# Optimization experiments

Measured on AMD Instinct MI355X. Metric: run time of the kernel, lower is better.

Reference implementation:

```python
import jax, jax.numpy as jnp
import numpy as np

B, CIN, COUT, H, W, K = 4, 3, 16, 256, 256, 5
PAD = K // 2  # replicate padding keeps spatial size


def _dilation_sum(x, w):
    """Learnable dilation, channel_merge_mode='sum'.
    x: (B,Cin,H,W), w: (Cout,Cin,K,K).
    out[b,o,i,j] = sum_c max_{di,dj} ( x_pad[b,c,i+di,j+dj] + w[o,c,di,dj] )
    """
    xp = jnp.pad(x, ((0, 0), (0, 0), (PAD, PAD), (PAD, PAD)), mode='edge')
    acc = jnp.full((x.shape[0], w.shape[0], x.shape[1], H, W), -jnp.inf, dtype=x.dtype)
    for di in range(K):  # fixed small kernel loop (unrolled), not a data-dim loop
        for dj in range(K):
            win = xp[:, :, di:di + H, dj:dj + W]                     # (B,Cin,H,W)
            cand = win[:, None] + w[None, :, :, di, dj][:, :, :, None, None]  # (B,Cout,Cin,H,W)
            acc = jnp.maximum(acc, cand)
    return acc.sum(axis=2)  # merge over input channels -> (B,Cout,H,W)


def _erosion_identity(y, w):
    """Learnable erosion, channel_merge_mode='identity' (each channel independent).
    y: (B,Cout,H,W), w: (Cout,K,K).
    out[b,o,i,j] = min_{di,dj} ( y_pad[b,o,i+di,j+dj] - w[o,di,dj] )
    """
    yp = jnp.pad(y, ((0, 0), (0, 0), (PAD, PAD), (PAD, PAD)), mode='edge')
    acc = jnp.full(y.shape, jnp.inf, dtype=y.dtype)
    for di in range(K):
        for dj in range(K):
            acc = jnp.minimum(acc, yp[:, :, di:di + H, dj:dj + W] - w[None, :, di, dj, None, None])
    return acc


def setup_inputs() -> dict:
    key = jax.random.key(0)
    k1, k2, k3 = jax.random.split(key, 3)
    x = jax.random.normal(k1, (B, CIN, H, W), dtype=jnp.float32)
    w_d = jax.random.normal(k2, (COUT, CIN, K, K), dtype=jnp.float32) * 0.05
    w_e = jax.random.normal(k3, (COUT, K, K), dtype=jnp.float32) * 0.05
    return {"x": x, "w_d": w_d, "w_e": w_e}


def reference(x, w_d, w_e):
    # Closing = dilation (max-plus, sum merge) followed by erosion (min-plus, identity merge)
    dilated = _dilation_sum(x, w_d)
    return _erosion_identity(dilated, w_e)
```

## Files before the change

kernel.cpp:

```cpp
#include <hip/hip_runtime.h>


namespace {
constexpr int Hh = 256, Ww = 256;
constexpr int CI = 3, CO = 16;
constexpr int TILE = 32;
constexpr int DT = 36;
constexpr int XT = 40;
}

__global__ __launch_bounds__(256, 4)
void closing_fused(const float* __restrict__ x, const float* __restrict__ wd,
                   const float* __restrict__ we, float* __restrict__ out) {
    __shared__ __align__(16) float sx[CI * XT * XT];
    __shared__ __align__(16) float sdil[DT * DT];

    const int tid = threadIdx.x;
    const int bx = blockIdx.x, by = blockIdx.y, z = blockIdx.z;
    const int o = z & 15;
    const int i0 = by * TILE, j0 = bx * TILE;

    const float* xb  = x + (size_t)(z >> 4) * (CI * Hh * Ww);
    const float* wdo = wd + o * (CI * 25);
    const float* weo = we + o * 25;

    for (int idx = tid; idx < CI * XT * XT; idx += 256) {
        const int c   = idx / (XT * XT);
        const int rem = idx - c * (XT * XT);
        const int r   = rem / XT;
        const int col = rem - r * XT;
        int gi = i0 - 4 + r;   gi = min(max(gi, 0), Hh - 1);
        int gj = j0 - 4 + col; gj = min(max(gj, 0), Ww - 1);
        sx[idx] = xb[c * (Hh * Ww) + gi * Ww + gj];
    }
    __syncthreads();

    for (int task = tid; task < DT * (DT / 4); task += 256) {
        const int tr = task / 9;
        const int tj = (task - tr * 9) * 4;
        float acc0 = 0.f, acc1 = 0.f, acc2 = 0.f, acc3 = 0.f;
#pragma unroll
        for (int c = 0; c < CI; ++c) {
            float win[5][8];
#pragma unroll
            for (int dd = 0; dd < 5; ++dd) {
                const float4 a  = *(const float4*)&sx[c*(XT*XT) + (tr+dd)*XT + tj];
                const float4 bq = *(const float4*)&sx[c*(XT*XT) + (tr+dd)*XT + tj + 4];
                win[dd][0]=a.x;  win[dd][1]=a.y;  win[dd][2]=a.z;  win[dd][3]=a.w;
                win[dd][4]=bq.x; win[dd][5]=bq.y; win[dd][6]=bq.z; win[dd][7]=bq.w;
            }
            float m0 = -3.402823e38f, m1 = m0, m2 = m0, m3 = m0;
#pragma unroll
            for (int dd = 0; dd < 5; ++dd) {
#pragma unroll
                for (int d2 = 0; d2 < 5; ++d2) {
                    const float wv = wdo[c*25 + dd*5 + d2];
                    m0 = fmaxf(m0, win[dd][d2+0] + wv);
                    m1 = fmaxf(m1, win[dd][d2+1] + wv);
                    m2 = fmaxf(m2, win[dd][d2+2] + wv);
                    m3 = fmaxf(m3, win[dd][d2+3] + wv);
                }
            }
            acc0 += m0; acc1 += m1; acc2 += m2; acc3 += m3;
        }
        *(float4*)&sdil[tr * DT + tj] = make_float4(acc0, acc1, acc2, acc3);
    }
    __syncthreads();

    const int r  = tid >> 3;
    const int oj = (tid & 7) * 4;
    float win[5][8];
    const bool interior = (bx != 0) & (bx != (Ww / TILE - 1)) &
                          (by != 0) & (by != (Hh / TILE - 1));
    if (interior) {
#pragma unroll
        for (int dd = 0; dd < 5; ++dd) {
            const float4 a  = *(const float4*)&sdil[(r+dd)*DT + oj];
            const float4 bq = *(const float4*)&sdil[(r+dd)*DT + oj + 4];
            win[dd][0]=a.x;  win[dd][1]=a.y;  win[dd][2]=a.z;  win[dd][3]=a.w;
            win[dd][4]=bq.x; win[dd][5]=bq.y; win[dd][6]=bq.z; win[dd][7]=bq.w;
        }
    } else {
        int lj[8];
#pragma unroll
        for (int m = 0; m < 8; ++m) {
            int g = j0 + oj + m - 2; g = min(max(g, 0), Ww - 1);
            lj[m] = g - j0 + 2;
        }
#pragma unroll
        for (int dd = 0; dd < 5; ++dd) {
            int g = i0 + r + dd - 2; g = min(max(g, 0), Hh - 1);
            const int li = g - i0 + 2;
#pragma unroll
            for (int m = 0; m < 8; ++m) win[dd][m] = sdil[li * DT + lj[m]];
        }
    }
    float r0 = 3.402823e38f, r1 = r0, r2 = r0, r3 = r0;
#pragma unroll
    for (int dd = 0; dd < 5; ++dd) {
#pragma unroll
        for (int d2 = 0; d2 < 5; ++d2) {
            const float wv = weo[dd*5 + d2];
            r0 = fminf(r0, win[dd][d2+0] - wv);
            r1 = fminf(r1, win[dd][d2+1] - wv);
            r2 = fminf(r2, win[dd][d2+2] - wv);
            r3 = fminf(r3, win[dd][d2+3] - wv);
        }
    }
    *(float4*)&out[((size_t)z << 16) + ((i0 + r) << 8) + (j0 + oj)] =
        make_float4(r0, r1, r2, r3);
}

extern "C" void kernel_launch(void* const* d_in, const int* in_sizes, int n_in,
                              void* d_out, int out_size, void* d_ws, size_t ws_size,
                              hipStream_t stream) {
    const float* x  = (const float*)d_in[0];
    const float* wd = (const float*)d_in[1];
    const float* we = (const float*)d_in[2];
    float* out = (float*)d_out;

    dim3 grid(Ww / TILE, Hh / TILE, 4 * CO);
    closing_fused<<<grid, dim3(256), 0, stream>>>(x, wd, we, out);
}
```

Baseline: 99.49 us.

## Widen tiles to 64x32, stream input channels, and precompute replicate borders in shared memory

Tiles become 64 columns by 32 rows, which cuts halo overhead. Input channels are loaded into shared memory one at a time instead of all three at once, which lowers shared-memory use and raises the occupancy hint to 6 blocks. Each thread now produces 8 dilation outputs per row. Replicate padding for the erosion is written into the dilated tile up front, so the separate clamped-index boundary path goes away. The costs are extra syncs per channel, higher register pressure from the 8-wide accumulators, and intricate edge-fixup logic.

```diff
diff --git a/kernel.cpp b/kernel.cpp
--- a/kernel.cpp
+++ b/kernel.cpp
@@ -1,114 +1,179 @@
 #include <hip/hip_runtime.h>
+#include <float.h>
 
 
 namespace {
-constexpr int Hh = 256, Ww = 256;
-constexpr int CI = 3, CO = 16;
-constexpr int TILE = 32;
-constexpr int DT = 36;
-constexpr int XT = 40;
+constexpr int HH = 256, WW = 256;
+constexpr int CI = 3;
+constexpr int TW = 64, TH = 32;
+constexpr int DW = 68, DH = 36;
+constexpr int XW = 76, XH = 40;
 }
 
-__global__ __launch_bounds__(256, 4)
-void closing_fused(const float* __restrict__ x, const float* __restrict__ wd,
-                   const float* __restrict__ we, float* __restrict__ out) {
-    __shared__ __align__(16) float sx[CI * XT * XT];
-    __shared__ __align__(16) float sdil[DT * DT];
+__global__ __launch_bounds__(256, 6)
+void closing_v2(const float* __restrict__ x, const float* __restrict__ wd,
+                const float* __restrict__ we, float* __restrict__ out) {
+    __shared__ __align__(16) float sx[XH * XW];
+    __shared__ __align__(16) float sdil[DH * DW];
 
     const int tid = threadIdx.x;
     const int bx = blockIdx.x, by = blockIdx.y, z = blockIdx.z;
-    const int o = z & 15;
-    const int i0 = by * TILE, j0 = bx * TILE;
+    const int o = z & 15, b = z >> 4;
+    const int i0 = by * TH, j0 = bx * TW;
+    const float* xb = x + (size_t)b * (CI * HH * WW);
 
-    const float* xb  = x + (size_t)(z >> 4) * (CI * Hh * Ww);
-    const float* wdo = wd + o * (CI * 25);
-    const float* weo = we + o * 25;
+    const int r0 = tid / 9, s0 = tid - r0 * 9;
+    const int t2 = tid + 256;
+    const int r1 = t2 / 9, s1 = t2 - r1 * 9;
+    const bool has2 = (t2 < DH * 9);
 
-    for (int idx = tid; idx < CI * XT * XT; idx += 256) {
-        const int c   = idx / (XT * XT);
-        const int rem = idx - c * (XT * XT);
-        const int r   = rem / XT;
-        const int col = rem - r * XT;
-        int gi = i0 - 4 + r;   gi = min(max(gi, 0), Hh - 1);
-        int gj = j0 - 4 + col; gj = min(max(gj, 0), Ww - 1);
-        sx[idx] = xb[c * (Hh * Ww) + gi * Ww + gj];
+    float acc0[8], acc1[8];
+#pragma unroll
+    for (int j = 0; j < 8; ++j) { acc0[j] = 0.f; acc1[j] = 0.f; }
+
+    for (int c = 0; c < CI; ++c) {
+        {
+            const float* xc = xb + c * (HH * WW);
+            int rs = tid / XW, cs = tid - rs * XW;
+#pragma unroll
+            for (int k = 0; k < 12; ++k) {
+                const int idx = tid + k * 256;
+                if (idx < XH * XW) {
+                    int gi = i0 - 4 + rs; gi = min(max(gi, 0), HH - 1);
+                    int gj = j0 - 4 + cs; gj = min(max(gj, 0), WW - 1);
+                    sx[idx] = xc[(gi << 8) + gj];
+                }
+                cs += 256 - 3 * XW;
+                rs += 3;
+                if (cs >= XW) { cs -= XW; rs += 1; }
+            }
+        }
+        __syncthreads();
+
+        const float* wr = wd + (o * CI + c) * 25;
+
+        {
+            float m[8];
+#pragma unroll
+            for (int j = 0; j < 8; ++j) m[j] = -FLT_MAX;
+#pragma unroll
+            for (int dd = 0; dd < 5; ++dd) {
+                const float* p = &sx[(r0 + dd) * XW + 8 * s0];
+                const float4 a  = *(const float4*)p;
+                const float4 bq = *(const float4*)(p + 4);
+                const float4 cq = *(const float4*)(p + 8);
+                const float win[12] = {a.x,a.y,a.z,a.w, bq.x,bq.y,bq.z,bq.w,
+                                       cq.x,cq.y,cq.z,cq.w};
+                const float w0 = wr[dd*5+0], w1 = wr[dd*5+1], w2 = wr[dd*5+2],
+                            w3 = wr[dd*5+3], w4 = wr[dd*5+4];
+#pragma unroll
+                for (int j = 0; j < 8; ++j) {
+                    m[j] = fmaxf(fmaxf(m[j], win[j]   + w0), win[j+1] + w1);
+                    m[j] = fmaxf(fmaxf(m[j], win[j+2] + w2), win[j+3] + w3);
+                    m[j] = fmaxf(m[j], win[j+4] + w4);
+                }
+            }
+#pragma unroll
+            for (int j = 0; j < 8; ++j) acc0[j] += m[j];
+        }
+        if (has2) {
+            float m[8];
+#pragma unroll
+            for (int j = 0; j < 8; ++j) m[j] = -FLT_MAX;
+#pragma unroll
+            for (int dd = 0; dd < 5; ++dd) {
+                const float* p = &sx[(r1 + dd) * XW + 8 * s1];
+                const float4 a  = *(const float4*)p;
+                const float4 bq = *(const float4*)(p + 4);
+                const float4 cq = *(const float4*)(p + 8);
+                const float win[12] = {a.x,a.y,a.z,a.w, bq.x,bq.y,bq.z,bq.w,
+                                       cq.x,cq.y,cq.z,cq.w};
+                const float w0 = wr[dd*5+0], w1 = wr[dd*5+1], w2 = wr[dd*5+2],
+                            w3 = wr[dd*5+3], w4 = wr[dd*5+4];
+#pragma unroll
+                for (int j = 0; j < 8; ++j) {
+                    m[j] = fmaxf(fmaxf(m[j], win[j]   + w0), win[j+1] + w1);
+                    m[j] = fmaxf(fmaxf(m[j], win[j+2] + w2), win[j+3] + w3);
+                    m[j] = fmaxf(m[j], win[j+4] + w4);
+                }
+            }
+#pragma unroll
+            for (int j = 0; j < 8; ++j) acc1[j] += m[j];
+        }
+        if (c < CI - 1) __syncthreads();
+    }
+
+    {
+        {
+            int r = r0, s = s0;
+            if (bx == 0 && s == 0) { acc0[0] = acc0[1] = acc0[2]; }
+            if (bx == 3 && s == 8) { acc0[2] = acc0[3] = acc0[1]; }
+            const bool shadow = (by == 0 && r < 2) || (by == 7 && r > 33);
+            if (!shadow) {
+                const float4 q0 = make_float4(acc0[0], acc0[1], acc0[2], acc0[3]);
+                const float4 q1 = make_float4(acc0[4], acc0[5], acc0[6], acc0[7]);
+                float* bp = &sdil[r * DW + 8 * s];
+                *(float4*)bp = q0; if (s < 8) *(float4*)(bp + 4) = q1;
+                if (by == 0 && r == 2) {
+                    *(float4*)&sdil[0*DW + 8*s] = q0; if (s<8) *(float4*)&sdil[0*DW + 8*s + 4] = q1;
+                    *(float4*)&sdil[1*DW + 8*s] = q0; if (s<8) *(float4*)&sdil[1*DW + 8*s + 4] = q1;
+                }
+                if (by == 7 && r == 33) {
+                    *(float4*)&sdil[34*DW + 8*s] = q0; if (s<8) *(float4*)&sdil[34*DW + 8*s + 4] = q1;
+                    *(float4*)&sdil[35*DW + 8*s] = q0; if (s<8) *(float4*)&sdil[35*DW + 8*s + 4] = q1;
+                }
+            }
+        }
+        if (has2) {
+            int r = r1, s = s1;
+            if (bx == 0 && s == 0) { acc1[0] = acc1[1] = acc1[2]; }
+            if (bx == 3 && s == 8) { acc1[2] = acc1[3] = acc1[1]; }
+            const bool shadow = (by == 0 && r < 2) || (by == 7 && r > 33);
+            if (!shadow) {
+                const float4 q0 = make_float4(acc1[0], acc1[1], acc1[2], acc1[3]);
+                const float4 q1 = make_float4(acc1[4], acc1[5], acc1[6], acc1[7]);
+                float* bp = &sdil[r * DW + 8 * s];
+                *(float4*)bp = q0; if (s < 8) *(float4*)(bp + 4) = q1;
+                if (by == 0 && r == 2) {
+                    *(float4*)&sdil[0*DW + 8*s] = q0; if (s<8) *(float4*)&sdil[0*DW + 8*s + 4] = q1;
+                    *(float4*)&sdil[1*DW + 8*s] = q0; if (s<8) *(float4*)&sdil[1*DW + 8*s + 4] = q1;
+                }
+                if (by == 7 && r == 33) {
+                    *(float4*)&sdil[34*DW + 8*s] = q0; if (s<8) *(float4*)&sdil[34*DW + 8*s + 4] = q1;
+                    *(float4*)&sdil[35*DW + 8*s] = q0; if (s<8) *(float4*)&sdil[35*DW + 8*s + 4] = q1;
+                }
+            }
+        }
     }
     __syncthreads();
 
-    for (int task = tid; task < DT * (DT / 4); task += 256) {
-        const int tr = task / 9;
-        const int tj = (task - tr * 9) * 4;
-        float acc0 = 0.f, acc1 = 0.f, acc2 = 0.f, acc3 = 0.f;
+    {
+        const int er = tid >> 3, es = tid & 7;
+        const float* ew = we + o * 25;
+        float rm[8];
 #pragma unroll
-        for (int c = 0; c < CI; ++c) {
-            float win[5][8];
-#pragma unroll
-            for (int dd = 0; dd < 5; ++dd) {
-                const float4 a  = *(const float4*)&sx[c*(XT*XT) + (tr+dd)*XT + tj];
-                const float4 bq = *(const float4*)&sx[c*(XT*XT) + (tr+dd)*XT + tj + 4];
-                win[dd][0]=a.x;  win[dd][1]=a.y;  win[dd][2]=a.z;  win[dd][3]=a.w;
-                win[dd][4]=bq.x; win[dd][5]=bq.y; win[dd][6]=bq.z; win[dd][7]=bq.w;
-            }
-            float m0 = -3.402823e38f, m1 = m0, m2 = m0, m3 = m0;
-#pragma unroll
-            for (int dd = 0; dd < 5; ++dd) {
-#pragma unroll
-                for (int d2 = 0; d2 < 5; ++d2) {
-                    const float wv = wdo[c*25 + dd*5 + d2];
-                    m0 = fmaxf(m0, win[dd][d2+0] + wv);
-                    m1 = fmaxf(m1, win[dd][d2+1] + wv);
-                    m2 = fmaxf(m2, win[dd][d2+2] + wv);
-                    m3 = fmaxf(m3, win[dd][d2+3] + wv);
-                }
-            }
-            acc0 += m0; acc1 += m1; acc2 += m2; acc3 += m3;
-        }
-        *(float4*)&sdil[tr * DT + tj] = make_float4(acc0, acc1, acc2, acc3);
-    }
-    __syncthreads();
-
-    const int r  = tid >> 3;
-    const int oj = (tid & 7) * 4;
-    float win[5][8];
-    const bool interior = (bx != 0) & (bx != (Ww / TILE - 1)) &
-                          (by != 0) & (by != (Hh / TILE - 1));
-    if (interior) {
+        for (int j = 0; j < 8; ++j) rm[j] = FLT_MAX;
 #pragma unroll
         for (int dd = 0; dd < 5; ++dd) {
-            const float4 a  = *(const float4*)&sdil[(r+dd)*DT + oj];
-            const float4 bq = *(const float4*)&sdil[(r+dd)*DT + oj + 4];
-            win[dd][0]=a.x;  win[dd][1]=a.y;  win[dd][2]=a.z;  win[dd][3]=a.w;
-            win[dd][4]=bq.x; win[dd][5]=bq.y; win[dd][6]=bq.z; win[dd][7]=bq.w;
+            const float* p = &sdil[(er + dd) * DW + 8 * es];
+            const float4 a  = *(const float4*)p;
+            const float4 bq = *(const float4*)(p + 4);
+            const float4 cq = *(const float4*)(p + 8);
+            const float win[12] = {a.x,a.y,a.z,a.w, bq.x,bq.y,bq.z,bq.w,
+                                   cq.x,cq.y,cq.z,cq.w};
+            const float e0 = ew[dd*5+0], e1 = ew[dd*5+1], e2 = ew[dd*5+2],
+                        e3 = ew[dd*5+3], e4 = ew[dd*5+4];
+#pragma unroll
+            for (int j = 0; j < 8; ++j) {
+                rm[j] = fminf(fminf(rm[j], win[j]   - e0), win[j+1] - e1);
+                rm[j] = fminf(fminf(rm[j], win[j+2] - e2), win[j+3] - e3);
+                rm[j] = fminf(rm[j], win[j+4] - e4);
+            }
         }
-    } else {
-        int lj[8];
-#pragma unroll
-        for (int m = 0; m < 8; ++m) {
-            int g = j0 + oj + m - 2; g = min(max(g, 0), Ww - 1);
-            lj[m] = g - j0 + 2;
-        }
-#pragma unroll
-        for (int dd = 0; dd < 5; ++dd) {
-            int g = i0 + r + dd - 2; g = min(max(g, 0), Hh - 1);
-            const int li = g - i0 + 2;
-#pragma unroll
-            for (int m = 0; m < 8; ++m) win[dd][m] = sdil[li * DT + lj[m]];
-        }
+        float* op = &out[((size_t)z << 16) + ((size_t)(i0 + er) << 8) + j0 + 8 * es];
+        *(float4*)op       = make_float4(rm[0], rm[1], rm[2], rm[3]);
+        *(float4*)(op + 4) = make_float4(rm[4], rm[5], rm[6], rm[7]);
     }
-    float r0 = 3.402823e38f, r1 = r0, r2 = r0, r3 = r0;
-#pragma unroll
-    for (int dd = 0; dd < 5; ++dd) {
-#pragma unroll
-        for (int d2 = 0; d2 < 5; ++d2) {
-            const float wv = weo[dd*5 + d2];
-            r0 = fminf(r0, win[dd][d2+0] - wv);
-            r1 = fminf(r1, win[dd][d2+1] - wv);
-            r2 = fminf(r2, win[dd][d2+2] - wv);
-            r3 = fminf(r3, win[dd][d2+3] - wv);
-        }
-    }
-    *(float4*)&out[((size_t)z << 16) + ((i0 + r) << 8) + (j0 + oj)] =
-        make_float4(r0, r1, r2, r3);
 }
 
 extern "C" void kernel_launch(void* const* d_in, const int* in_sizes, int n_in,
@@ -119,6 +184,6 @@
     const float* we = (const float*)d_in[2];
     float* out = (float*)d_out;
 
-    dim3 grid(Ww / TILE, Hh / TILE, 4 * CO);
-    closing_fused<<<grid, dim3(256), 0, stream>>>(x, wd, we, out);
+    dim3 grid(WW / TW, HH / TH, 4 * 16);
+    closing_v2<<<grid, dim3(256), 0, stream>>>(x, wd, we, out);
 }
```

After: 170.8 us. 71.7% more time.

## Use 4x4 register tiles for dilation and fold edge replication into stores

Applied to the files above, without the earlier changes.

The dilation stage now has each of 81 threads compute a 4x4 output block, reading 8 shared-memory rows once and reusing them across four output rows instead of reloading a 5x8 window per row. The erosion's replicate-padding branch is removed by writing clamped duplicate values into the dilated tile's border cells during the dilation store. Erosion is done by 128 threads producing 8 outputs each. Shared-memory row strides are padded to 44. The cost is that only 81 and 128 of 256 threads are busy in the two compute stages, which lowers parallelism per block.

```diff
diff --git a/kernel.cpp b/kernel.cpp
--- a/kernel.cpp
+++ b/kernel.cpp
@@ -1,114 +1,125 @@
 #include <hip/hip_runtime.h>
+#include <float.h>
 
 
 namespace {
-constexpr int Hh = 256, Ww = 256;
-constexpr int CI = 3, CO = 16;
-constexpr int TILE = 32;
-constexpr int DT = 36;
-constexpr int XT = 40;
+constexpr int HH = 256, WW = 256, CI = 3;
+constexpr int TT = 32;
+constexpr int DS = 44;
+constexpr int XS = 44;
+constexpr int XR = 40;
+constexpr int XCH = XR * XS;
+}
+
+__device__ __forceinline__ float4 dapp(float4 m, float4 A, float4 B,
+                                       float w0, float w1, float w2, float w3, float w4) {
+    m.x = fmaxf(fmaxf(fmaxf(m.x, A.x + w0), fmaxf(A.y + w1, A.z + w2)), fmaxf(A.w + w3, B.x + w4));
+    m.y = fmaxf(fmaxf(fmaxf(m.y, A.y + w0), fmaxf(A.z + w1, A.w + w2)), fmaxf(B.x + w3, B.y + w4));
+    m.z = fmaxf(fmaxf(fmaxf(m.z, A.z + w0), fmaxf(A.w + w1, B.x + w2)), fmaxf(B.y + w3, B.z + w4));
+    m.w = fmaxf(fmaxf(fmaxf(m.w, A.w + w0), fmaxf(B.x + w1, B.y + w2)), fmaxf(B.z + w3, B.w + w4));
+    return m;
+}
+
+__device__ __forceinline__ void add4(float4& a, float4 m) {
+    a.x += m.x; a.y += m.y; a.z += m.z; a.w += m.w;
 }
 
 __global__ __launch_bounds__(256, 4)
-void closing_fused(const float* __restrict__ x, const float* __restrict__ wd,
-                   const float* __restrict__ we, float* __restrict__ out) {
-    __shared__ __align__(16) float sx[CI * XT * XT];
-    __shared__ __align__(16) float sdil[DT * DT];
+void closing_v3(const float* __restrict__ x, const float* __restrict__ wd,
+                const float* __restrict__ we, float* __restrict__ out) {
+    __shared__ __align__(16) float sx[CI * XCH];
+    __shared__ __align__(16) float sdil[36 * DS];
 
     const int tid = threadIdx.x;
     const int bx = blockIdx.x, by = blockIdx.y, z = blockIdx.z;
-    const int o = z & 15;
-    const int i0 = by * TILE, j0 = bx * TILE;
+    const int o = z & 15, b = z >> 4;
+    const int i0 = by * TT, j0 = bx * TT;
+    const float* xb = x + (size_t)b * (CI * HH * WW);
 
-    const float* xb  = x + (size_t)(z >> 4) * (CI * Hh * Ww);
-    const float* wdo = wd + o * (CI * 25);
-    const float* weo = we + o * 25;
-
-    for (int idx = tid; idx < CI * XT * XT; idx += 256) {
-        const int c   = idx / (XT * XT);
-        const int rem = idx - c * (XT * XT);
-        const int r   = rem / XT;
-        const int col = rem - r * XT;
-        int gi = i0 - 4 + r;   gi = min(max(gi, 0), Hh - 1);
-        int gj = j0 - 4 + col; gj = min(max(gj, 0), Ww - 1);
-        sx[idx] = xb[c * (Hh * Ww) + gi * Ww + gj];
+#pragma unroll
+    for (int k = 0; k < 19; ++k) {
+        const int idx = tid + (k << 8);
+        if (idx < CI * XR * XR) {
+            const int c   = idx / 1600;
+            const int rem = idx - c * 1600;
+            const int rr  = rem / 40;
+            const int cc  = rem - rr * 40;
+            int gi = i0 - 4 + rr; gi = min(max(gi, 0), HH - 1);
+            int gj = j0 - 4 + cc; gj = min(max(gj, 0), WW - 1);
+            sx[c * XCH + rr * XS + cc] = xb[c * (HH * WW) + (gi << 8) + gj];
+        }
     }
     __syncthreads();
 
-    for (int task = tid; task < DT * (DT / 4); task += 256) {
-        const int tr = task / 9;
-        const int tj = (task - tr * 9) * 4;
-        float acc0 = 0.f, acc1 = 0.f, acc2 = 0.f, acc3 = 0.f;
+    if (tid < 81) {
+        const int q = tid / 9, s = tid - q * 9;
+        float4 acc0 = {0,0,0,0}, acc1 = acc0, acc2 = acc0, acc3 = acc0;
 #pragma unroll
         for (int c = 0; c < CI; ++c) {
-            float win[5][8];
+            const float* wr = wd + (o * CI + c) * 25;
+            const float* base = &sx[c * XCH + (4 * q) * XS + 4 * s];
+            const float NEG = -FLT_MAX;
+            float4 m0 = {NEG,NEG,NEG,NEG}, m1 = m0, m2 = m0, m3 = m0;
 #pragma unroll
-            for (int dd = 0; dd < 5; ++dd) {
-                const float4 a  = *(const float4*)&sx[c*(XT*XT) + (tr+dd)*XT + tj];
-                const float4 bq = *(const float4*)&sx[c*(XT*XT) + (tr+dd)*XT + tj + 4];
-                win[dd][0]=a.x;  win[dd][1]=a.y;  win[dd][2]=a.z;  win[dd][3]=a.w;
-                win[dd][4]=bq.x; win[dd][5]=bq.y; win[dd][6]=bq.z; win[dd][7]=bq.w;
+            for (int dd = 0; dd < 8; ++dd) {
+                const float4 A = *(const float4*)(base + dd * XS);
+                const float4 B = *(const float4*)(base + dd * XS + 4);
+                if (dd <= 4)           m0 = dapp(m0, A, B, wr[dd*5+0], wr[dd*5+1], wr[dd*5+2], wr[dd*5+3], wr[dd*5+4]);
+                if (dd >= 1 && dd <= 5){ const int k2 = dd-1;
+                                       m1 = dapp(m1, A, B, wr[k2*5+0], wr[k2*5+1], wr[k2*5+2], wr[k2*5+3], wr[k2*5+4]); }
+                if (dd >= 2 && dd <= 6){ const int k2 = dd-2;
+                                       m2 = dapp(m2, A, B, wr[k2*5+0], wr[k2*5+1], wr[k2*5+2], wr[k2*5+3], wr[k2*5+4]); }
+                if (dd >= 3)           { const int k2 = dd-3;
+                                       m3 = dapp(m3, A, B, wr[k2*5+0], wr[k2*5+1], wr[k2*5+2], wr[k2*5+3], wr[k2*5+4]); }
             }
-            float m0 = -3.402823e38f, m1 = m0, m2 = m0, m3 = m0;
-#pragma unroll
-            for (int dd = 0; dd < 5; ++dd) {
-#pragma unroll
-                for (int d2 = 0; d2 < 5; ++d2) {
-                    const float wv = wdo[c*25 + dd*5 + d2];
-                    m0 = fmaxf(m0, win[dd][d2+0] + wv);
-                    m1 = fmaxf(m1, win[dd][d2+1] + wv);
-                    m2 = fmaxf(m2, win[dd][d2+2] + wv);
-                    m3 = fmaxf(m3, win[dd][d2+3] + wv);
-                }
-            }
-            acc0 += m0; acc1 += m1; acc2 += m2; acc3 += m3;
+            add4(acc0, m0); add4(acc1, m1); add4(acc2, m2); add4(acc3, m3);
         }
-        *(float4*)&sdil[tr * DT + tj] = make_float4(acc0, acc1, acc2, acc3);
+
+        if (bx == 0 && s == 0) {
+            acc0.x = acc0.y = acc0.z;  acc1.x = acc1.y = acc1.z;
+            acc2.x = acc2.y = acc2.z;  acc3.x = acc3.y = acc3.z;
+        }
+        if (bx == 7 && s == 8) {
+            acc0.z = acc0.w = acc0.y;  acc1.z = acc1.w = acc1.y;
+            acc2.z = acc2.w = acc2.y;  acc3.z = acc3.w = acc3.y;
+        }
+        float4 w0 = acc0, w1 = acc1, w2 = acc2, w3 = acc3;
+        if (by == 0 && q == 0) { w0 = acc2; w1 = acc2; }
+        if (by == 7 && q == 8) { w2 = acc1; w3 = acc1; }
+        float* dp = &sdil[(4 * q) * DS + 4 * s];
+        *(float4*)(dp)          = w0;
+        *(float4*)(dp + DS)     = w1;
+        *(float4*)(dp + 2 * DS) = w2;
+        *(float4*)(dp + 3 * DS) = w3;
     }
     __syncthreads();
 
-    const int r  = tid >> 3;
-    const int oj = (tid & 7) * 4;
-    float win[5][8];
-    const bool interior = (bx != 0) & (bx != (Ww / TILE - 1)) &
-                          (by != 0) & (by != (Hh / TILE - 1));
-    if (interior) {
+    if (tid < 128) {
+        const int s = tid & 3, r = tid >> 2;
+        const float* ew = we + o * 25;
+        const float* eb = &sdil[r * DS + 8 * s];
+        const float PF = FLT_MAX;
+        float4 r0 = {PF,PF,PF,PF}, r1 = r0;
 #pragma unroll
         for (int dd = 0; dd < 5; ++dd) {
-            const float4 a  = *(const float4*)&sdil[(r+dd)*DT + oj];
-            const float4 bq = *(const float4*)&sdil[(r+dd)*DT + oj + 4];
-            win[dd][0]=a.x;  win[dd][1]=a.y;  win[dd][2]=a.z;  win[dd][3]=a.w;
-            win[dd][4]=bq.x; win[dd][5]=bq.y; win[dd][6]=bq.z; win[dd][7]=bq.w;
+            const float4 A = *(const float4*)(eb + dd * DS);
+            const float4 B = *(const float4*)(eb + dd * DS + 4);
+            const float4 C = *(const float4*)(eb + dd * DS + 8);
+            const float e0 = ew[dd*5+0], e1 = ew[dd*5+1], e2 = ew[dd*5+2],
+                        e3 = ew[dd*5+3], e4 = ew[dd*5+4];
+            r0.x = fminf(fminf(fminf(r0.x, A.x - e0), fminf(A.y - e1, A.z - e2)), fminf(A.w - e3, B.x - e4));
+            r0.y = fminf(fminf(fminf(r0.y, A.y - e0), fminf(A.z - e1, A.w - e2)), fminf(B.x - e3, B.y - e4));
+            r0.z = fminf(fminf(fminf(r0.z, A.z - e0), fminf(A.w - e1, B.x - e2)), fminf(B.y - e3, B.z - e4));
+            r0.w = fminf(fminf(fminf(r0.w, A.w - e0), fminf(B.x - e1, B.y - e2)), fminf(B.z - e3, B.w - e4));
+            r1.x = fminf(fminf(fminf(r1.x, B.x - e0), fminf(B.y - e1, B.z - e2)), fminf(B.w - e3, C.x - e4));
+            r1.y = fminf(fminf(fminf(r1.y, B.y - e0), fminf(B.z - e1, B.w - e2)), fminf(C.x - e3, C.y - e4));
+            r1.z = fminf(fminf(fminf(r1.z, B.z - e0), fminf(B.w - e1, C.x - e2)), fminf(C.y - e3, C.z - e4));
+            r1.w = fminf(fminf(fminf(r1.w, B.w - e0), fminf(C.x - e1, C.y - e2)), fminf(C.z - e3, C.w - e4));
         }
-    } else {
-        int lj[8];
-#pragma unroll
-        for (int m = 0; m < 8; ++m) {
-            int g = j0 + oj + m - 2; g = min(max(g, 0), Ww - 1);
-            lj[m] = g - j0 + 2;
-        }
-#pragma unroll
-        for (int dd = 0; dd < 5; ++dd) {
-            int g = i0 + r + dd - 2; g = min(max(g, 0), Hh - 1);
-            const int li = g - i0 + 2;
-#pragma unroll
-            for (int m = 0; m < 8; ++m) win[dd][m] = sdil[li * DT + lj[m]];
-        }
+        float* op = &out[((size_t)z << 16) + ((size_t)(i0 + r) << 8) + j0 + 8 * s];
+        *(float4*)op       = r0;
+        *(float4*)(op + 4) = r1;
     }
-    float r0 = 3.402823e38f, r1 = r0, r2 = r0, r3 = r0;
-#pragma unroll
-    for (int dd = 0; dd < 5; ++dd) {
-#pragma unroll
-        for (int d2 = 0; d2 < 5; ++d2) {
-            const float wv = weo[dd*5 + d2];
-            r0 = fminf(r0, win[dd][d2+0] - wv);
-            r1 = fminf(r1, win[dd][d2+1] - wv);
-            r2 = fminf(r2, win[dd][d2+2] - wv);
-            r3 = fminf(r3, win[dd][d2+3] - wv);
-        }
-    }
-    *(float4*)&out[((size_t)z << 16) + ((i0 + r) << 8) + (j0 + oj)] =
-        make_float4(r0, r1, r2, r3);
 }
 
 extern "C" void kernel_launch(void* const* d_in, const int* in_sizes, int n_in,
@@ -119,6 +130,6 @@
     const float* we = (const float*)d_in[2];
     float* out = (float*)d_out;
 
-    dim3 grid(Ww / TILE, Hh / TILE, 4 * CO);
-    closing_fused<<<grid, dim3(256), 0, stream>>>(x, wd, we, out);
+    dim3 grid(WW / TT, HH / TT, 4 * 16);
+    closing_v3<<<grid, dim3(256), 0, stream>>>(x, wd, we, out);
 }
```

Result: slower. 110.1 us (+10.7%).
